# Optimization experiments

Measured on AMD Instinct MI355X. Metric: run time of the kernel, lower is better.

## Reference

```python
import jax, jax.numpy as jnp
import numpy as np

NUM_HEADS = 16
NUM_KV_HEADS = 4
HEAD_DIM = 128
SCALE = 0.08838834764831845  # 1/sqrt(128)
BATCH = 4
SEQLEN = 1024
TOTAL = BATCH * SEQLEN


def setup_inputs() -> dict:
    key = jax.random.key(0)
    kq, kk, kv = jax.random.split(key, 3)
    q = jax.random.normal(kq, (TOTAL, NUM_HEADS, HEAD_DIM), dtype=jnp.float32)
    k = jax.random.normal(kk, (TOTAL, NUM_KV_HEADS, HEAD_DIM), dtype=jnp.float32)
    v = jax.random.normal(kv, (TOTAL, NUM_KV_HEADS, HEAD_DIM), dtype=jnp.float32)
    cu = jnp.arange(BATCH + 1, dtype=jnp.int32) * SEQLEN  # [0,1024,2048,3072,4096]
    return {"q": q, "k": k, "v": v, "cu_seqlens_q": cu, "cu_seqlens_k": cu}


def reference(q, k, v, cu_seqlens_q, cu_seqlens_k):
    # Prefill varlen causal attention (block_tables=None, empty kv cache).
    # Equal-length segments -> reshape packed tokens to [B, S, H, D].
    B = cu_seqlens_q.shape[0] - 1
    S = q.shape[0] // B
    H, Dh = q.shape[1], q.shape[2]
    Hkv = k.shape[1]
    g = H // Hkv  # GQA group size

    qb = q.reshape(B, S, H, Dh)
    # repeat_interleave kv heads to match query heads
    kb = jnp.repeat(k.reshape(B, S, Hkv, Dh), g, axis=2)  # [B,S,H,Dh]
    vb = jnp.repeat(v.reshape(B, S, Hkv, Dh), g, axis=2)

    scores = jnp.einsum('bqhd,bkhd->bhqk', qb, kb) * SCALE  # [B,H,S,S]
    causal = jnp.tril(jnp.ones((S, S), dtype=bool))
    scores = jnp.where(causal, scores, jnp.finfo(scores.dtype).min)
    probs = jax.nn.softmax(scores, axis=-1)
    o = jnp.einsum('bhqk,bkhd->bqhd', probs, vb)  # [B,S,H,Dh]
    return o.reshape(B * S, H, Dh)
```

## Files before the change

### kernel.cpp

```cpp
#include <hip/hip_runtime.h>
#include <cstddef>

#define NH 16
#define NKV 4
#define HD 128
#define SEQ 1024
#define SCALE_F 0.08838834764831845f
#define QSCALE 0.12751743f

typedef __attribute__((ext_vector_type(8))) short short8;
typedef __attribute__((ext_vector_type(4))) float floatx4;

union F8 { short8 v; unsigned short u[8]; };

__device__ __forceinline__ unsigned short f2bf(float f) {
  unsigned int u = __float_as_uint(f);
  u += 0x7FFFu + ((u >> 16) & 1u);
  return (unsigned short)(u >> 16);
}

__device__ __forceinline__ unsigned int pk_bf16(float lo, float hi) {
  unsigned int r;
  asm("v_cvt_pk_bf16_f32 %0, %1, %2" : "=v"(r) : "v"(lo), "v"(hi));
  return r;
}

__device__ __forceinline__ void glds16(const void* g, void* l) {
  __builtin_amdgcn_global_load_lds(
      (const __attribute__((address_space(1))) unsigned int*)g,
      (__attribute__((address_space(3))) unsigned int*)l, 16, 0, 0);
}

__global__ __launch_bounds__(256) void prepass(const float* __restrict__ kg,
                                               const float* __restrict__ vg,
                                               unsigned short* __restrict__ Ktg,
                                               unsigned short* __restrict__ Vtg) {
  __shared__ float Vl[32 * 132];
  const int tid = threadIdx.x;
  const int bid = blockIdx.x;
  if (bid < 512) {
    const int bkvh = bid >> 5, tile = bid & 31;
    const int b = bkvh >> 2, kvh = bkvh & 3;
    const int kpos = tid >> 3;
    const int d8base = (tid & 7) * 2;
    const size_t tok = (size_t)b * SEQ + tile * 32 + kpos;
    const float* src = kg + (tok * NKV + kvh) * HD + d8base * 8;
    unsigned short* dstT = Ktg + (size_t)bid * 4096;
#pragma unroll
    for (int i = 0; i < 2; ++i) {
      floatx4 a = ((const floatx4*)src)[0];
      floatx4 c = ((const floatx4*)src)[1];
      F8 t;
#pragma unroll
      for (int j = 0; j < 4; ++j) { t.u[j] = f2bf(a[j]); t.u[4 + j] = f2bf(c[j]); }
      const int blk = kpos * 16 + ((d8base + i) ^ (kpos & 15));
      *(short8*)(dstT + blk * 8) = t.v;
      src += 8;
    }
  } else {
    const int bb = bid - 512;
    const int bkvh = bb >> 5, tile = bb & 31;
    const int b = bkvh >> 2, kvh = bkvh & 3;
    const int r = tid >> 3;
    const int c16 = (tid & 7) * 16;
    const size_t tok = (size_t)b * SEQ + tile * 32 + r;
    const float* src = vg + (tok * NKV + kvh) * HD + c16;
#pragma unroll
    for (int j = 0; j < 4; ++j)
      *(floatx4*)&Vl[r * 132 + c16 + j * 4] = ((const floatx4*)src)[j];
    __syncthreads();
    unsigned short* dstT = Vtg + (size_t)bb * 4096;
#pragma unroll
    for (int i = 0; i < 2; ++i) {
      const int o = tid * 2 + i;
      const int d = o >> 2, s8 = o & 3;
      F8 t;
#pragma unroll
      for (int j = 0; j < 8; ++j) {
        const int s = s8 * 8 + j;
        const int k = (s >> 1) + ((s & 1) << 4);
        t.u[j] = f2bf(Vl[k * 132 + d]);
      }
      const int blk = d * 4 + (s8 ^ (d & 3));
      *(short8*)(dstT + blk * 8) = t.v;
    }
  }
}

__global__ __launch_bounds__(256, 4)
void fa_fwd7(const float* __restrict__ qg, const unsigned short* __restrict__ Ktg,
             const unsigned short* __restrict__ Vtg, float* __restrict__ og) {
  __shared__ __align__(16) unsigned short Kb[2][4096];
  __shared__ __align__(16) unsigned int Pb[4][16 * 20];

  const int tid = threadIdx.x;
  const int wave = tid >> 6;
  const int lane = tid & 63;
  const int col = lane & 15;
  const int quad = lane >> 4;

  const int idx = blockIdx.x;
  const int g = idx >> 8;
  const int u = (idx >> 6) & 3;
  const int bh = idx & 63;
  const int qt = g * 4 + ((u + g) & 3);
  const int h = bh & 15;
  const int b = bh >> 4;
  const int kvh = h >> 2;
  const int seg = b * SEQ;
  const int wq0 = qt * 64 + wave * 16;
  const int tb = (b * NKV + kvh) * 32;

  F8 qf[4];
  {
    const float* qp = qg + ((size_t)(seg + wq0 + col) * NH + h) * HD + quad * 8;
#pragma unroll
    for (int ks = 0; ks < 4; ++ks) {
      floatx4 a = ((const floatx4*)(qp + ks * 32))[0];
      floatx4 c = ((const floatx4*)(qp + ks * 32))[1];
#pragma unroll
      for (int j = 0; j < 4; ++j) {
        qf[ks].u[j] = f2bf(a[j] * QSCALE);
        qf[ks].u[4 + j] = f2bf(c[j] * QSCALE);
      }
    }
  }

  floatx4 acc[8];
#pragma unroll
  for (int dt = 0; dt < 8; ++dt) acc[dt] = (floatx4){0.f, 0.f, 0.f, 0.f};
  float lsum[4] = {0.f, 0.f, 0.f, 0.f};

  const int nkt = 2 * (qt + 1);
  const int stoff = wave * 2048 + lane * 16;

  {
    const char* gK = (const char*)Ktg + (size_t)tb * 8192 + stoff;
    char* lK = (char*)&Kb[0][0] + wave * 2048;
    glds16(gK, lK);
    glds16(gK + 1024, lK + 1024);
  }
  __syncthreads();

  for (int kt = 0; kt < nkt; ++kt) {
    const int cb = kt & 1, nb = cb ^ 1;
    const int kbase = kt * 32;
    const bool act = (kbase <= wq0 + 15);

    F8 vr[8];
    if (act) {
      const unsigned short* Vt = Vtg + (size_t)(tb + kt) * 4096;
#pragma unroll
      for (int dt = 0; dt < 8; ++dt)
        vr[dt].v = *(const short8*)&Vt[((dt * 16 + col) * 4 + (quad ^ (col & 3))) * 8];
    }

    if (kt + 1 < nkt) {
      const char* gK = (const char*)Ktg + (size_t)(tb + kt + 1) * 8192 + stoff;
      char* lK = (char*)&Kb[nb][0] + wave * 2048;
      glds16(gK, lK);
      glds16(gK + 1024, lK + 1024);
    }

    if (act) {
      floatx4 s0 = {0.f, 0.f, 0.f, 0.f}, s1 = {0.f, 0.f, 0.f, 0.f};
#pragma unroll
      for (int ks = 0; ks < 4; ++ks) {
        F8 k0, k1;
        k0.v = *(const short8*)&Kb[cb][(col * 16 + ((ks * 4 + quad) ^ col)) * 8];
        k1.v = *(const short8*)&Kb[cb][((16 + col) * 16 + ((ks * 4 + quad) ^ col)) * 8];
        s0 = __builtin_amdgcn_mfma_f32_16x16x32_bf16(qf[ks].v, k0.v, s0, 0, 0, 0);
        s1 = __builtin_amdgcn_mfma_f32_16x16x32_bf16(qf[ks].v, k1.v, s1, 0, 0, 0);
      }
      const bool diag = (kbase + 31 > wq0);
#pragma unroll
      for (int r = 0; r < 4; ++r) {
        float p0 = __builtin_amdgcn_exp2f(s0[r]);
        float p1 = __builtin_amdgcn_exp2f(s1[r]);
        if (diag) {
          const int q0 = wq0 + quad * 4 + r;
          p0 = (kbase + col > q0) ? 0.f : p0;
          p1 = (kbase + 16 + col > q0) ? 0.f : p1;
        }
        lsum[r] += p0 + p1;
        Pb[wave][(quad * 4 + r) * 20 + col] = pk_bf16(p0, p1);
      }
      F8 pa;
      pa.v = *(const short8*)&Pb[wave][col * 20 + quad * 4];
#pragma unroll
      for (int dt = 0; dt < 8; ++dt)
        acc[dt] = __builtin_amdgcn_mfma_f32_16x16x32_bf16(pa.v, vr[dt].v, acc[dt], 0, 0, 0);
    }
    __syncthreads();
  }

#pragma unroll
  for (int r = 0; r < 4; ++r) {
    float l = lsum[r];
    l += __shfl_xor(l, 1);
    l += __shfl_xor(l, 2);
    l += __shfl_xor(l, 4);
    l += __shfl_xor(l, 8);
    const float inv = 1.0f / l;
    float* op = og + ((size_t)(seg + wq0 + quad * 4 + r) * NH + h) * HD;
#pragma unroll
    for (int dt = 0; dt < 8; ++dt) op[dt * 16 + col] = acc[dt][r] * inv;
  }
}

#define KST 136
#define VST 40
#define PST 40

__global__ __launch_bounds__(256, 2)
void fa_fwd(const float* __restrict__ qg, const float* __restrict__ kg,
            const float* __restrict__ vg, float* __restrict__ og) {
  __shared__ unsigned short Klds[32 * KST];
  __shared__ unsigned short Vt[HD * VST];
  __shared__ unsigned short Pl[4][32 * PST];

  const int tid = threadIdx.x;
  const int wave = tid >> 6;
  const int lane = tid & 63;
  const int col = lane & 15;
  const int quad = lane >> 4;

  const int idx = blockIdx.x;
  const int raw = idx & 7;
  const int qt = (idx & 256) ? raw : 7 - raw;
  const int bh = idx >> 3;
  const int h = bh & 15;
  const int b = bh >> 4;
  const int kvh = h >> 2;
  const int seg = b * SEQ;
  const int wq0 = qt * 128 + wave * 32;

  F8 qf[2][4];
#pragma unroll
  for (int mt = 0; mt < 2; ++mt) {
    const size_t qrow = (size_t)(seg + wq0 + mt * 16 + col);
    const float* qp = qg + (qrow * NH + h) * HD + quad * 8;
#pragma unroll
    for (int ks = 0; ks < 4; ++ks) {
      const floatx4* p4 = (const floatx4*)(qp + ks * 32);
      floatx4 a = p4[0], c = p4[1];
#pragma unroll
      for (int j = 0; j < 4; ++j) {
        qf[mt][ks].u[j] = f2bf(a[j] * SCALE_F);
        qf[mt][ks].u[4 + j] = f2bf(c[j] * SCALE_F);
      }
    }
  }

  floatx4 acc[2][8];
#pragma unroll
  for (int mt = 0; mt < 2; ++mt)
#pragma unroll
    for (int dt = 0; dt < 8; ++dt)
      acc[mt][dt] = (floatx4){0.f, 0.f, 0.f, 0.f};
  float lsum[2][4];
#pragma unroll
  for (int mt = 0; mt < 2; ++mt)
#pragma unroll
    for (int r = 0; r < 4; ++r) lsum[mt][r] = 0.f;

  const int nkt = 4 * (qt + 1);
  const int sr = tid >> 3;
  const int sc = (tid & 7) * 16;

  for (int kt = 0; kt < nkt; ++kt) {
    const int kbase = kt * 32;
    __syncthreads();
    {
      const size_t tok = (size_t)(seg + kbase + sr);
      const floatx4* kp4 = (const floatx4*)(kg + (tok * NKV + kvh) * HD + sc);
      floatx4 kv0 = kp4[0], kv1 = kp4[1], kv2 = kp4[2], kv3 = kp4[3];
      float kf32[16] = {kv0[0],kv0[1],kv0[2],kv0[3], kv1[0],kv1[1],kv1[2],kv1[3],
                        kv2[0],kv2[1],kv2[2],kv2[3], kv3[0],kv3[1],kv3[2],kv3[3]};
      unsigned int* dst = (unsigned int*)&Klds[sr * KST + sc];
#pragma unroll
      for (int j = 0; j < 8; ++j)
        dst[j] = (unsigned int)f2bf(kf32[2 * j]) | ((unsigned int)f2bf(kf32[2 * j + 1]) << 16);
      const floatx4* vp4 = (const floatx4*)(vg + (tok * NKV + kvh) * HD + sc);
      floatx4 vv0 = vp4[0], vv1 = vp4[1], vv2 = vp4[2], vv3 = vp4[3];
      unsigned short vb[16] = {
        f2bf(vv0[0]),f2bf(vv0[1]),f2bf(vv0[2]),f2bf(vv0[3]),
        f2bf(vv1[0]),f2bf(vv1[1]),f2bf(vv1[2]),f2bf(vv1[3]),
        f2bf(vv2[0]),f2bf(vv2[1]),f2bf(vv2[2]),f2bf(vv2[3]),
        f2bf(vv3[0]),f2bf(vv3[1]),f2bf(vv3[2]),f2bf(vv3[3])};
#pragma unroll
      for (int s = 0; s < 16; ++s) {
        int j = (s + tid) & 15;
        Vt[(sc + j) * VST + sr] = vb[j];
      }
    }
    __syncthreads();

    if (kbase > wq0 + 31) continue;

    F8 kf[4][2];
#pragma unroll
    for (int ks = 0; ks < 4; ++ks)
#pragma unroll
      for (int nt = 0; nt < 2; ++nt)
        kf[ks][nt].v = *(const short8*)&Klds[(nt * 16 + col) * KST + ks * 32 + quad * 8];

#pragma unroll
    for (int mt = 0; mt < 2; ++mt) {
      floatx4 s0 = {0.f, 0.f, 0.f, 0.f}, s1 = {0.f, 0.f, 0.f, 0.f};
#pragma unroll
      for (int ks = 0; ks < 4; ++ks) {
        s0 = __builtin_amdgcn_mfma_f32_16x16x32_bf16(qf[mt][ks].v, kf[ks][0].v, s0, 0, 0, 0);
        s1 = __builtin_amdgcn_mfma_f32_16x16x32_bf16(qf[mt][ks].v, kf[ks][1].v, s1, 0, 0, 0);
      }
      const int q0 = wq0 + mt * 16 + quad * 4;
      const bool diag = (kbase + 31 > wq0 + mt * 16);
      unsigned short* pw = &Pl[wave][(mt * 16 + quad * 4) * PST];
#pragma unroll
      for (int r = 0; r < 4; ++r) {
        float p0 = __expf(s0[r]);
        float p1 = __expf(s1[r]);
        if (diag) {
          p0 = (kbase + col > q0 + r) ? 0.f : p0;
          p1 = (kbase + 16 + col > q0 + r) ? 0.f : p1;
        }
        lsum[mt][r] += p0 + p1;
        pw[r * PST + col] = f2bf(p0);
        pw[r * PST + 16 + col] = f2bf(p1);
      }
    }
    F8 pa[2];
#pragma unroll
    for (int mt = 0; mt < 2; ++mt)
      pa[mt].v = *(const short8*)&Pl[wave][(mt * 16 + col) * PST + quad * 8];
#pragma unroll
    for (int dt = 0; dt < 8; ++dt) {
      F8 vb;
      vb.v = *(const short8*)&Vt[(dt * 16 + col) * VST + quad * 8];
#pragma unroll
      for (int mt = 0; mt < 2; ++mt)
        acc[mt][dt] = __builtin_amdgcn_mfma_f32_16x16x32_bf16(pa[mt].v, vb.v, acc[mt][dt], 0, 0, 0);
    }
  }

#pragma unroll
  for (int mt = 0; mt < 2; ++mt) {
#pragma unroll
    for (int r = 0; r < 4; ++r) {
      float l = lsum[mt][r];
      l += __shfl_xor(l, 1);
      l += __shfl_xor(l, 2);
      l += __shfl_xor(l, 4);
      l += __shfl_xor(l, 8);
      const float inv = 1.0f / l;
      const int qi = wq0 + mt * 16 + quad * 4 + r;
      float* op = og + ((size_t)(seg + qi) * NH + h) * HD;
#pragma unroll
      for (int dt = 0; dt < 8; ++dt)
        op[dt * 16 + col] = acc[mt][dt][r] * inv;
    }
  }
}

extern "C" void kernel_launch(void* const* d_in, const int* in_sizes, int n_in,
                              void* d_out, int out_size, void* d_ws, size_t ws_size,
                              hipStream_t stream) {
  const float* q = (const float*)d_in[0];
  const float* k = (const float*)d_in[1];
  const float* v = (const float*)d_in[2];
  float* out = (float*)d_out;
  if (ws_size >= (size_t)(8 * 1024 * 1024)) {
    unsigned short* Ktg = (unsigned short*)d_ws;
    unsigned short* Vtg = Ktg + 2097152;
    hipLaunchKernelGGL(prepass, dim3(1024), dim3(256), 0, stream, k, v, Ktg, Vtg);
    hipLaunchKernelGGL(fa_fwd7, dim3(1024), dim3(256), 0, stream, q, Ktg, Vtg, out);
  } else {
    hipLaunchKernelGGL(fa_fwd, dim3(512), dim3(256), 0, stream, q, k, v, out);
  }
}
```

Measured before the change: 129.1 us.

## Split long causal query tiles across two blocks with a normalization pass

Adds a split-K variant in which query tiles 8-15 are each handled by two blocks covering halves of the key range. Partial unnormalized outputs and row sums go to workspace, and a separate kernel combines and normalizes them. The goal is to balance per-block work under the causal mask and add more blocks for better occupancy. In exchange it needs extra global traffic for the partials, a third kernel launch, and a larger workspace requirement, so it only runs when the workspace is at least 26 MB.

```diff
diff --git a/kernel.cpp b/kernel.cpp
--- a/kernel.cpp
+++ b/kernel.cpp
@@ -88,6 +88,176 @@
 }
 
 __global__ __launch_bounds__(256, 4)
+void fa_fwd9(const float* __restrict__ qg, const unsigned short* __restrict__ Ktg,
+             const unsigned short* __restrict__ Vtg, float* __restrict__ og,
+             float* __restrict__ Pacc, float* __restrict__ Ls0,
+             float* __restrict__ Ls1) {
+  __shared__ __align__(16) unsigned short Kb[2][4096];
+  __shared__ __align__(16) unsigned int Pb[4][16 * 20];
+
+  const int tid = threadIdx.x;
+  const int wave = tid >> 6;
+  const int lane = tid & 63;
+  const int col = lane & 15;
+  const int quad = lane >> 4;
+
+  const int idx = blockIdx.x;
+  const int bh = idx & 63;
+  const int j = idx >> 6;
+  const int h = bh & 15;
+  const int b = bh >> 4;
+  const int kvh = h >> 2;
+  const int seg = b * SEQ;
+  const int tb = (b * NKV + kvh) * 32;
+
+  int qt, k0, k1, mode;
+  if (j < 8) {
+    qt = j; k0 = 0; k1 = 2 * (qt + 1); mode = 0;
+  } else {
+    const int s = j - 8;
+    qt = 8 + (s >> 1);
+    if ((s & 1) == 0) { k0 = 0;      k1 = qt + 1;       mode = 1; }
+    else              { k0 = qt + 1; k1 = 2 * (qt + 1); mode = 2; }
+  }
+  const int wq0 = qt * 64 + wave * 16;
+
+  F8 qf[4];
+  {
+    const float* qp = qg + ((size_t)(seg + wq0 + col) * NH + h) * HD + quad * 8;
+#pragma unroll
+    for (int ks = 0; ks < 4; ++ks) {
+      floatx4 a = ((const floatx4*)(qp + ks * 32))[0];
+      floatx4 c = ((const floatx4*)(qp + ks * 32))[1];
+#pragma unroll
+      for (int jj = 0; jj < 4; ++jj) {
+        qf[ks].u[jj] = f2bf(a[jj] * QSCALE);
+        qf[ks].u[4 + jj] = f2bf(c[jj] * QSCALE);
+      }
+    }
+  }
+
+  floatx4 acc[8];
+#pragma unroll
+  for (int dt = 0; dt < 8; ++dt) acc[dt] = (floatx4){0.f, 0.f, 0.f, 0.f};
+  float lsum[4] = {0.f, 0.f, 0.f, 0.f};
+
+  const int stoff = wave * 2048 + lane * 16;
+
+  {
+    const char* gK = (const char*)Ktg + (size_t)(tb + k0) * 8192 + stoff;
+    char* lK = (char*)&Kb[0][0] + wave * 2048;
+    glds16(gK, lK);
+    glds16(gK + 1024, lK + 1024);
+  }
+  __syncthreads();
+
+  for (int kt = k0; kt < k1; ++kt) {
+    const int cb = (kt - k0) & 1, nb = cb ^ 1;
+    const int kbase = kt * 32;
+    const bool act = (kbase <= wq0 + 15);
+
+    F8 vr[8];
+    if (act) {
+      const unsigned short* Vt = Vtg + (size_t)(tb + kt) * 4096;
+#pragma unroll
+      for (int dt = 0; dt < 8; ++dt)
+        vr[dt].v = *(const short8*)&Vt[((dt * 16 + col) * 4 + (quad ^ (col & 3))) * 8];
+    }
+
+    if (kt + 1 < k1) {
+      const char* gK = (const char*)Ktg + (size_t)(tb + kt + 1) * 8192 + stoff;
+      char* lK = (char*)&Kb[nb][0] + wave * 2048;
+      glds16(gK, lK);
+      glds16(gK + 1024, lK + 1024);
+    }
+
+    if (act) {
+      floatx4 s0 = {0.f, 0.f, 0.f, 0.f}, s1 = {0.f, 0.f, 0.f, 0.f};
+#pragma unroll
+      for (int ks = 0; ks < 4; ++ks) {
+        F8 kk0, kk1;
+        kk0.v = *(const short8*)&Kb[cb][(col * 16 + ((ks * 4 + quad) ^ col)) * 8];
+        kk1.v = *(const short8*)&Kb[cb][((16 + col) * 16 + ((ks * 4 + quad) ^ col)) * 8];
+        s0 = __builtin_amdgcn_mfma_f32_16x16x32_bf16(qf[ks].v, kk0.v, s0, 0, 0, 0);
+        s1 = __builtin_amdgcn_mfma_f32_16x16x32_bf16(qf[ks].v, kk1.v, s1, 0, 0, 0);
+      }
+      const bool diag = (kbase + 31 > wq0);
+#pragma unroll
+      for (int r = 0; r < 4; ++r) {
+        float p0 = __builtin_amdgcn_exp2f(s0[r]);
+        float p1 = __builtin_amdgcn_exp2f(s1[r]);
+        if (diag) {
+          const int q0 = wq0 + quad * 4 + r;
+          p0 = (kbase + col > q0) ? 0.f : p0;
+          p1 = (kbase + 16 + col > q0) ? 0.f : p1;
+        }
+        lsum[r] += p0 + p1;
+        Pb[wave][(quad * 4 + r) * 20 + col] = pk_bf16(p0, p1);
+      }
+      F8 pa;
+      pa.v = *(const short8*)&Pb[wave][col * 20 + quad * 4];
+#pragma unroll
+      for (int dt = 0; dt < 8; ++dt)
+        acc[dt] = __builtin_amdgcn_mfma_f32_16x16x32_bf16(pa.v, vr[dt].v, acc[dt], 0, 0, 0);
+    }
+    __syncthreads();
+  }
+
+#pragma unroll
+  for (int r = 0; r < 4; ++r) {
+    float l = lsum[r];
+    l += __shfl_xor(l, 1);
+    l += __shfl_xor(l, 2);
+    l += __shfl_xor(l, 4);
+    l += __shfl_xor(l, 8);
+    if (mode == 0) {
+      const float inv = 1.0f / l;
+      float* op = og + ((size_t)(seg + wq0 + quad * 4 + r) * NH + h) * HD;
+#pragma unroll
+      for (int dt = 0; dt < 8; ++dt) op[dt * 16 + col] = acc[dt][r] * inv;
+    } else {
+      const int roff = (qt - 8) * 64 + wave * 16 + quad * 4 + r;
+      const int lrow = (b * NH + h) * 512 + roff;
+      if (mode == 1) {
+        float* pp = Pacc + (size_t)lrow * 128;
+#pragma unroll
+        for (int dt = 0; dt < 8; ++dt) pp[dt * 16 + col] = acc[dt][r];
+        if (col == 0) Ls0[lrow] = l;
+      } else {
+        float* op = og + ((size_t)(seg + wq0 + quad * 4 + r) * NH + h) * HD;
+#pragma unroll
+        for (int dt = 0; dt < 8; ++dt) op[dt * 16 + col] = acc[dt][r];
+        if (col == 0) Ls1[lrow] = l;
+      }
+    }
+  }
+}
+
+__global__ __launch_bounds__(256)
+void norm_k(float* __restrict__ og, const float* __restrict__ Pacc,
+            const float* __restrict__ Ls0, const float* __restrict__ Ls1) {
+  const int t = blockIdx.x * 256 + threadIdx.x;
+  const int e = t * 8;
+  const int lrow = e >> 7;
+  const int d = e & 127;
+  const float inv = 1.0f / (Ls0[lrow] + Ls1[lrow]);
+  const int b = lrow >> 13;
+  const int rem = lrow & 8191;
+  const int h = rem >> 9;
+  const int roff = rem & 511;
+  float* op = og + (((size_t)(b * 1024 + 512 + roff) * NH + h) * HD + d);
+  const float* pp = Pacc + (size_t)lrow * 128 + d;
+#pragma unroll
+  for (int i = 0; i < 2; ++i) {
+    floatx4 o = ((floatx4*)op)[i];
+    floatx4 p = ((const floatx4*)pp)[i];
+#pragma unroll
+    for (int k = 0; k < 4; ++k) o[k] = (o[k] + p[k]) * inv;
+    ((floatx4*)op)[i] = o;
+  }
+}
+
+__global__ __launch_bounds__(256, 4)
 void fa_fwd7(const float* __restrict__ qg, const unsigned short* __restrict__ Ktg,
              const unsigned short* __restrict__ Vtg, float* __restrict__ og) {
   __shared__ __align__(16) unsigned short Kb[2][4096];
@@ -119,9 +289,9 @@
       floatx4 a = ((const floatx4*)(qp + ks * 32))[0];
       floatx4 c = ((const floatx4*)(qp + ks * 32))[1];
 #pragma unroll
-      for (int j = 0; j < 4; ++j) {
-        qf[ks].u[j] = f2bf(a[j] * QSCALE);
-        qf[ks].u[4 + j] = f2bf(c[j] * QSCALE);
+      for (int jj = 0; jj < 4; ++jj) {
+        qf[ks].u[jj] = f2bf(a[jj] * QSCALE);
+        qf[ks].u[4 + jj] = f2bf(c[jj] * QSCALE);
       }
     }
   }
@@ -166,11 +336,11 @@
       floatx4 s0 = {0.f, 0.f, 0.f, 0.f}, s1 = {0.f, 0.f, 0.f, 0.f};
 #pragma unroll
       for (int ks = 0; ks < 4; ++ks) {
-        F8 k0, k1;
-        k0.v = *(const short8*)&Kb[cb][(col * 16 + ((ks * 4 + quad) ^ col)) * 8];
-        k1.v = *(const short8*)&Kb[cb][((16 + col) * 16 + ((ks * 4 + quad) ^ col)) * 8];
-        s0 = __builtin_amdgcn_mfma_f32_16x16x32_bf16(qf[ks].v, k0.v, s0, 0, 0, 0);
-        s1 = __builtin_amdgcn_mfma_f32_16x16x32_bf16(qf[ks].v, k1.v, s1, 0, 0, 0);
+        F8 kk0, kk1;
+        kk0.v = *(const short8*)&Kb[cb][(col * 16 + ((ks * 4 + quad) ^ col)) * 8];
+        kk1.v = *(const short8*)&Kb[cb][((16 + col) * 16 + ((ks * 4 + quad) ^ col)) * 8];
+        s0 = __builtin_amdgcn_mfma_f32_16x16x32_bf16(qf[ks].v, kk0.v, s0, 0, 0, 0);
+        s1 = __builtin_amdgcn_mfma_f32_16x16x32_bf16(qf[ks].v, kk1.v, s1, 0, 0, 0);
       }
       const bool diag = (kbase + 31 > wq0);
 #pragma unroll
@@ -245,9 +415,9 @@
       const floatx4* p4 = (const floatx4*)(qp + ks * 32);
       floatx4 a = p4[0], c = p4[1];
 #pragma unroll
-      for (int j = 0; j < 4; ++j) {
-        qf[mt][ks].u[j] = f2bf(a[j] * SCALE_F);
-        qf[mt][ks].u[4 + j] = f2bf(c[j] * SCALE_F);
+      for (int jj = 0; jj < 4; ++jj) {
+        qf[mt][ks].u[jj] = f2bf(a[jj] * SCALE_F);
+        qf[mt][ks].u[4 + jj] = f2bf(c[jj] * SCALE_F);
       }
     }
   }
@@ -279,8 +449,8 @@
                         kv2[0],kv2[1],kv2[2],kv2[3], kv3[0],kv3[1],kv3[2],kv3[3]};
       unsigned int* dst = (unsigned int*)&Klds[sr * KST + sc];
 #pragma unroll
-      for (int j = 0; j < 8; ++j)
-        dst[j] = (unsigned int)f2bf(kf32[2 * j]) | ((unsigned int)f2bf(kf32[2 * j + 1]) << 16);
+      for (int jj = 0; jj < 8; ++jj)
+        dst[jj] = (unsigned int)f2bf(kf32[2 * jj]) | ((unsigned int)f2bf(kf32[2 * jj + 1]) << 16);
       const floatx4* vp4 = (const floatx4*)(vg + (tok * NKV + kvh) * HD + sc);
       floatx4 vv0 = vp4[0], vv1 = vp4[1], vv2 = vp4[2], vv3 = vp4[3];
       unsigned short vb[16] = {
@@ -290,8 +460,8 @@
         f2bf(vv3[0]),f2bf(vv3[1]),f2bf(vv3[2]),f2bf(vv3[3])};
 #pragma unroll
       for (int s = 0; s < 16; ++s) {
-        int j = (s + tid) & 15;
-        Vt[(sc + j) * VST + sr] = vb[j];
+        int jj = (s + tid) & 15;
+        Vt[(sc + jj) * VST + sr] = vb[jj];
       }
     }
     __syncthreads();
@@ -369,7 +539,18 @@
   const float* k = (const float*)d_in[1];
   const float* v = (const float*)d_in[2];
   float* out = (float*)d_out;
-  if (ws_size >= (size_t)(8 * 1024 * 1024)) {
+  const size_t MB = 1024 * 1024;
+  if (ws_size >= 26 * MB) {
+    unsigned short* Ktg = (unsigned short*)d_ws;
+    unsigned short* Vtg = Ktg + 2097152;
+    float* Pacc = (float*)((char*)d_ws + 8 * MB);
+    float* Ls0 = (float*)((char*)d_ws + 24 * MB);
+    float* Ls1 = Ls0 + 32768;
+    hipLaunchKernelGGL(prepass, dim3(1024), dim3(256), 0, stream, k, v, Ktg, Vtg);
+    hipLaunchKernelGGL(fa_fwd9, dim3(1536), dim3(256), 0, stream, q, Ktg, Vtg,
+                       out, Pacc, Ls0, Ls1);
+    hipLaunchKernelGGL(norm_k, dim3(2048), dim3(256), 0, stream, out, Pacc, Ls0, Ls1);
+  } else if (ws_size >= 8 * MB) {
     unsigned short* Ktg = (unsigned short*)d_ws;
     unsigned short* Vtg = Ktg + 2097152;
     hipLaunchKernelGGL(prepass, dim3(1024), dim3(256), 0, stream, k, v, Ktg, Vtg);
```

New measurement: 139.8 us. 8.3% more time.

## Read K fragments directly from global memory, dropping LDS staging and block barriers

Applied to the files above, without the earlier changes.

The main attention kernel stops staging K tiles into double-buffered shared memory through global_load_lds. Each wave now loads its K MFMA fragments straight from the pre-swizzled bf16 workspace, and V as before. Because waves no longer share a buffer, the per-iteration __syncthreads is removed and each wave runs only as many key tiles as its own causal rows need. This also skips the idle barrier iterations of early waves. The trade-off is that every wave reads K from global memory or cache separately instead of once per block, so K traffic rises and load latency is no longer overlapped through a prefetch.

```diff
diff --git a/kernel.cpp b/kernel.cpp
--- a/kernel.cpp
+++ b/kernel.cpp
@@ -23,12 +23,6 @@
   unsigned int r;
   asm("v_cvt_pk_bf16_f32 %0, %1, %2" : "=v"(r) : "v"(lo), "v"(hi));
   return r;
-}
-
-__device__ __forceinline__ void glds16(const void* g, void* l) {
-  __builtin_amdgcn_global_load_lds(
-      (const __attribute__((address_space(1))) unsigned int*)g,
-      (__attribute__((address_space(3))) unsigned int*)l, 16, 0, 0);
 }
 
 __global__ __launch_bounds__(256) void prepass(const float* __restrict__ kg,
@@ -88,9 +82,8 @@
 }
 
 __global__ __launch_bounds__(256, 4)
-void fa_fwd7(const float* __restrict__ qg, const unsigned short* __restrict__ Ktg,
-             const unsigned short* __restrict__ Vtg, float* __restrict__ og) {
-  __shared__ __align__(16) unsigned short Kb[2][4096];
+void fa_fwd10(const float* __restrict__ qg, const unsigned short* __restrict__ Ktg,
+              const unsigned short* __restrict__ Vtg, float* __restrict__ og) {
   __shared__ __align__(16) unsigned int Pb[4][16 * 20];
 
   const int tid = threadIdx.x;
@@ -131,67 +124,50 @@
   for (int dt = 0; dt < 8; ++dt) acc[dt] = (floatx4){0.f, 0.f, 0.f, 0.f};
   float lsum[4] = {0.f, 0.f, 0.f, 0.f};
 
-  const int nkt = 2 * (qt + 1);
-  const int stoff = wave * 2048 + lane * 16;
-
-  {
-    const char* gK = (const char*)Ktg + (size_t)tb * 8192 + stoff;
-    char* lK = (char*)&Kb[0][0] + wave * 2048;
-    glds16(gK, lK);
-    glds16(gK + 1024, lK + 1024);
-  }
-  __syncthreads();
-
-  for (int kt = 0; kt < nkt; ++kt) {
-    const int cb = kt & 1, nb = cb ^ 1;
+  const int nktw = ((wq0 + 15) >> 5) + 1;
+
+  int koff[4];
+#pragma unroll
+  for (int ks = 0; ks < 4; ++ks) koff[ks] = (col * 16 + ((ks * 4 + quad) ^ col)) * 8;
+  const int voffbase = (quad ^ (col & 3)) * 8;
+
+  for (int kt = 0; kt < nktw; ++kt) {
     const int kbase = kt * 32;
-    const bool act = (kbase <= wq0 + 15);
+    const unsigned short* Kt = Ktg + (size_t)(tb + kt) * 4096;
+    const unsigned short* Vt = Vtg + (size_t)(tb + kt) * 4096;
 
     F8 vr[8];
-    if (act) {
-      const unsigned short* Vt = Vtg + (size_t)(tb + kt) * 4096;
-#pragma unroll
-      for (int dt = 0; dt < 8; ++dt)
-        vr[dt].v = *(const short8*)&Vt[((dt * 16 + col) * 4 + (quad ^ (col & 3))) * 8];
-    }
-
-    if (kt + 1 < nkt) {
-      const char* gK = (const char*)Ktg + (size_t)(tb + kt + 1) * 8192 + stoff;
-      char* lK = (char*)&Kb[nb][0] + wave * 2048;
-      glds16(gK, lK);
-      glds16(gK + 1024, lK + 1024);
-    }
-
-    if (act) {
-      floatx4 s0 = {0.f, 0.f, 0.f, 0.f}, s1 = {0.f, 0.f, 0.f, 0.f};
-#pragma unroll
-      for (int ks = 0; ks < 4; ++ks) {
-        F8 k0, k1;
-        k0.v = *(const short8*)&Kb[cb][(col * 16 + ((ks * 4 + quad) ^ col)) * 8];
-        k1.v = *(const short8*)&Kb[cb][((16 + col) * 16 + ((ks * 4 + quad) ^ col)) * 8];
-        s0 = __builtin_amdgcn_mfma_f32_16x16x32_bf16(qf[ks].v, k0.v, s0, 0, 0, 0);
-        s1 = __builtin_amdgcn_mfma_f32_16x16x32_bf16(qf[ks].v, k1.v, s1, 0, 0, 0);
-      }
-      const bool diag = (kbase + 31 > wq0);
-#pragma unroll
-      for (int r = 0; r < 4; ++r) {
-        float p0 = __builtin_amdgcn_exp2f(s0[r]);
-        float p1 = __builtin_amdgcn_exp2f(s1[r]);
-        if (diag) {
-          const int q0 = wq0 + quad * 4 + r;
-          p0 = (kbase + col > q0) ? 0.f : p0;
-          p1 = (kbase + 16 + col > q0) ? 0.f : p1;
-        }
-        lsum[r] += p0 + p1;
-        Pb[wave][(quad * 4 + r) * 20 + col] = pk_bf16(p0, p1);
-      }
-      F8 pa;
-      pa.v = *(const short8*)&Pb[wave][col * 20 + quad * 4];
-#pragma unroll
-      for (int dt = 0; dt < 8; ++dt)
-        acc[dt] = __builtin_amdgcn_mfma_f32_16x16x32_bf16(pa.v, vr[dt].v, acc[dt], 0, 0, 0);
-    }
-    __syncthreads();
+#pragma unroll
+    for (int dt = 0; dt < 8; ++dt)
+      vr[dt].v = *(const short8*)&Vt[(dt * 16 + col) * 32 + voffbase];
+
+    floatx4 s0 = {0.f, 0.f, 0.f, 0.f}, s1 = {0.f, 0.f, 0.f, 0.f};
+#pragma unroll
+    for (int ks = 0; ks < 4; ++ks) {
+      F8 k0, k1;
+      k0.v = *(const short8*)&Kt[koff[ks]];
+      k1.v = *(const short8*)&Kt[16 * 16 * 8 + koff[ks]];
+      s0 = __builtin_amdgcn_mfma_f32_16x16x32_bf16(qf[ks].v, k0.v, s0, 0, 0, 0);
+      s1 = __builtin_amdgcn_mfma_f32_16x16x32_bf16(qf[ks].v, k1.v, s1, 0, 0, 0);
+    }
+    const bool diag = (kbase + 31 > wq0);
+#pragma unroll
+    for (int r = 0; r < 4; ++r) {
+      float p0 = __builtin_amdgcn_exp2f(s0[r]);
+      float p1 = __builtin_amdgcn_exp2f(s1[r]);
+      if (diag) {
+        const int q0 = wq0 + quad * 4 + r;
+        p0 = (kbase + col > q0) ? 0.f : p0;
+        p1 = (kbase + 16 + col > q0) ? 0.f : p1;
+      }
+      lsum[r] += p0 + p1;
+      Pb[wave][(quad * 4 + r) * 20 + col] = pk_bf16(p0, p1);
+    }
+    F8 pa;
+    pa.v = *(const short8*)&Pb[wave][col * 20 + quad * 4];
+#pragma unroll
+    for (int dt = 0; dt < 8; ++dt)
+      acc[dt] = __builtin_amdgcn_mfma_f32_16x16x32_bf16(pa.v, vr[dt].v, acc[dt], 0, 0, 0);
   }
 
 #pragma unroll
@@ -245,9 +221,9 @@
       const floatx4* p4 = (const floatx4*)(qp + ks * 32);
       floatx4 a = p4[0], c = p4[1];
 #pragma unroll
-      for (int j = 0; j < 4; ++j) {
-        qf[mt][ks].u[j] = f2bf(a[j] * SCALE_F);
-        qf[mt][ks].u[4 + j] = f2bf(c[j] * SCALE_F);
+      for (int jj = 0; jj < 4; ++jj) {
+        qf[mt][ks].u[jj] = f2bf(a[jj] * SCALE_F);
+        qf[mt][ks].u[4 + jj] = f2bf(c[jj] * SCALE_F);
       }
     }
   }
@@ -279,8 +255,8 @@
                         kv2[0],kv2[1],kv2[2],kv2[3], kv3[0],kv3[1],kv3[2],kv3[3]};
       unsigned int* dst = (unsigned int*)&Klds[sr * KST + sc];
 #pragma unroll
-      for (int j = 0; j < 8; ++j)
-        dst[j] = (unsigned int)f2bf(kf32[2 * j]) | ((unsigned int)f2bf(kf32[2 * j + 1]) << 16);
+      for (int jj = 0; jj < 8; ++jj)
+        dst[jj] = (unsigned int)f2bf(kf32[2 * jj]) | ((unsigned int)f2bf(kf32[2 * jj + 1]) << 16);
       const floatx4* vp4 = (const floatx4*)(vg + (tok * NKV + kvh) * HD + sc);
       floatx4 vv0 = vp4[0], vv1 = vp4[1], vv2 = vp4[2], vv3 = vp4[3];
       unsigned short vb[16] = {
@@ -290,8 +266,8 @@
         f2bf(vv3[0]),f2bf(vv3[1]),f2bf(vv3[2]),f2bf(vv3[3])};
 #pragma unroll
       for (int s = 0; s < 16; ++s) {
-        int j = (s + tid) & 15;
-        Vt[(sc + j) * VST + sr] = vb[j];
+        int jj = (s + tid) & 15;
+        Vt[(sc + jj) * VST + sr] = vb[jj];
       }
     }
     __syncthreads();
@@ -373,7 +349,7 @@
     unsigned short* Ktg = (unsigned short*)d_ws;
     unsigned short* Vtg = Ktg + 2097152;
     hipLaunchKernelGGL(prepass, dim3(1024), dim3(256), 0, stream, k, v, Ktg, Vtg);
-    hipLaunchKernelGGL(fa_fwd7, dim3(1024), dim3(256), 0, stream, q, Ktg, Vtg, out);
+    hipLaunchKernelGGL(fa_fwd10, dim3(1024), dim3(256), 0, stream, q, Ktg, Vtg, out);
   } else {
     hipLaunchKernelGGL(fa_fwd, dim3(512), dim3(256), 0, stream, q, k, v, out);
   }
```

Result: slower. 154.5 us (+19.7%).

## Process two 16-row query tiles per wave to reuse K/V fragments

Applied to the files above, without the earlier changes.

Each wave now handles 32 query rows as two 16-row sub-tiles, A and B. The K fragments read from LDS and the V fragments read from global memory are shared between both sub-tiles, so the block covers 128 query rows and the grid is halved to 512 blocks. The block-to-tile mapping changes to interleave even and odd super-tiles for causal load balance. The cost is doubled accumulator and register pressure, and launch bounds drop to 2 blocks per SM, which lowers occupancy.

```diff
diff --git a/kernel.cpp b/kernel.cpp
--- a/kernel.cpp
+++ b/kernel.cpp
@@ -87,11 +87,12 @@
   }
 }
 
-__global__ __launch_bounds__(256, 4)
-void fa_fwd7(const float* __restrict__ qg, const unsigned short* __restrict__ Ktg,
-             const unsigned short* __restrict__ Vtg, float* __restrict__ og) {
+__global__ __launch_bounds__(256, 2)
+void fa_fwd11(const float* __restrict__ qg, const unsigned short* __restrict__ Ktg,
+              const unsigned short* __restrict__ Vtg, float* __restrict__ og) {
   __shared__ __align__(16) unsigned short Kb[2][4096];
-  __shared__ __align__(16) unsigned int Pb[4][16 * 20];
+  __shared__ __align__(16) unsigned int PbA[4][320];
+  __shared__ __align__(16) unsigned int PbB[4][320];
 
   const int tid = threadIdx.x;
   const int wave = tid >> 6;
@@ -100,103 +101,139 @@
   const int quad = lane >> 4;
 
   const int idx = blockIdx.x;
-  const int g = idx >> 8;
-  const int u = (idx >> 6) & 3;
   const int bh = idx & 63;
-  const int qt = g * 4 + ((u + g) & 3);
+  const int st = (idx < 256) ? 2 * (idx >> 6) : 2 * ((idx - 256) >> 6) + 1;
   const int h = bh & 15;
   const int b = bh >> 4;
   const int kvh = h >> 2;
   const int seg = b * SEQ;
-  const int wq0 = qt * 64 + wave * 16;
+  const int wq0 = st * 128 + wave * 32;
   const int tb = (b * NKV + kvh) * 32;
-
-  F8 qf[4];
+  const int nkt = 4 * (st + 1);
+
+  F8 qfA[4], qfB[4];
   {
-    const float* qp = qg + ((size_t)(seg + wq0 + col) * NH + h) * HD + quad * 8;
+    const float* qpA = qg + ((size_t)(seg + wq0 + col) * NH + h) * HD + quad * 8;
+    const float* qpB = qg + ((size_t)(seg + wq0 + 16 + col) * NH + h) * HD + quad * 8;
 #pragma unroll
     for (int ks = 0; ks < 4; ++ks) {
-      floatx4 a = ((const floatx4*)(qp + ks * 32))[0];
-      floatx4 c = ((const floatx4*)(qp + ks * 32))[1];
+      floatx4 a = ((const floatx4*)(qpA + ks * 32))[0];
+      floatx4 c = ((const floatx4*)(qpA + ks * 32))[1];
 #pragma unroll
       for (int j = 0; j < 4; ++j) {
-        qf[ks].u[j] = f2bf(a[j] * QSCALE);
-        qf[ks].u[4 + j] = f2bf(c[j] * QSCALE);
-      }
-    }
-  }
-
-  floatx4 acc[8];
-#pragma unroll
-  for (int dt = 0; dt < 8; ++dt) acc[dt] = (floatx4){0.f, 0.f, 0.f, 0.f};
-  float lsum[4] = {0.f, 0.f, 0.f, 0.f};
-
-  const int nkt = 2 * (qt + 1);
+        qfA[ks].u[j] = f2bf(a[j] * QSCALE);
+        qfA[ks].u[4 + j] = f2bf(c[j] * QSCALE);
+      }
+      a = ((const floatx4*)(qpB + ks * 32))[0];
+      c = ((const floatx4*)(qpB + ks * 32))[1];
+#pragma unroll
+      for (int j = 0; j < 4; ++j) {
+        qfB[ks].u[j] = f2bf(a[j] * QSCALE);
+        qfB[ks].u[4 + j] = f2bf(c[j] * QSCALE);
+      }
+    }
+  }
+
+  floatx4 accA[8], accB[8];
+#pragma unroll
+  for (int dt = 0; dt < 8; ++dt) {
+    accA[dt] = (floatx4){0.f, 0.f, 0.f, 0.f};
+    accB[dt] = (floatx4){0.f, 0.f, 0.f, 0.f};
+  }
+  float lsumA[4] = {0.f, 0.f, 0.f, 0.f};
+  float lsumB[4] = {0.f, 0.f, 0.f, 0.f};
+
   const int stoff = wave * 2048 + lane * 16;
 
-  {
-    const char* gK = (const char*)Ktg + (size_t)tb * 8192 + stoff;
-    char* lK = (char*)&Kb[0][0] + wave * 2048;
-    glds16(gK, lK);
-    glds16(gK + 1024, lK + 1024);
-  }
+#define STAGE(T, BUF)                                                       \
+  do {                                                                      \
+    const char* gK_ = (const char*)Ktg + (size_t)(tb + (T)) * 8192 + stoff; \
+    char* lK_ = (char*)&Kb[BUF][0] + wave * 2048;                           \
+    glds16(gK_, lK_);                                                       \
+    glds16(gK_ + 1024, lK_ + 1024);                                         \
+  } while (0)
+
+  STAGE(0, 0);
   __syncthreads();
 
   for (int kt = 0; kt < nkt; ++kt) {
     const int cb = kt & 1, nb = cb ^ 1;
     const int kbase = kt * 32;
-    const bool act = (kbase <= wq0 + 15);
+    const bool actA = (kbase <= wq0 + 15);
+    const bool actB = (kbase <= wq0 + 31);
 
     F8 vr[8];
-    if (act) {
+    if (actB) {
       const unsigned short* Vt = Vtg + (size_t)(tb + kt) * 4096;
 #pragma unroll
       for (int dt = 0; dt < 8; ++dt)
         vr[dt].v = *(const short8*)&Vt[((dt * 16 + col) * 4 + (quad ^ (col & 3))) * 8];
     }
 
-    if (kt + 1 < nkt) {
-      const char* gK = (const char*)Ktg + (size_t)(tb + kt + 1) * 8192 + stoff;
-      char* lK = (char*)&Kb[nb][0] + wave * 2048;
-      glds16(gK, lK);
-      glds16(gK + 1024, lK + 1024);
-    }
-
-    if (act) {
-      floatx4 s0 = {0.f, 0.f, 0.f, 0.f}, s1 = {0.f, 0.f, 0.f, 0.f};
+    if (kt + 1 < nkt) STAGE(kt + 1, nb);
+
+    if (actB) {
+      floatx4 sA0 = {0.f, 0.f, 0.f, 0.f}, sA1 = {0.f, 0.f, 0.f, 0.f};
+      floatx4 sB0 = {0.f, 0.f, 0.f, 0.f}, sB1 = {0.f, 0.f, 0.f, 0.f};
 #pragma unroll
       for (int ks = 0; ks < 4; ++ks) {
         F8 k0, k1;
         k0.v = *(const short8*)&Kb[cb][(col * 16 + ((ks * 4 + quad) ^ col)) * 8];
         k1.v = *(const short8*)&Kb[cb][((16 + col) * 16 + ((ks * 4 + quad) ^ col)) * 8];
-        s0 = __builtin_amdgcn_mfma_f32_16x16x32_bf16(qf[ks].v, k0.v, s0, 0, 0, 0);
-        s1 = __builtin_amdgcn_mfma_f32_16x16x32_bf16(qf[ks].v, k1.v, s1, 0, 0, 0);
-      }
-      const bool diag = (kbase + 31 > wq0);
-#pragma unroll
-      for (int r = 0; r < 4; ++r) {
-        float p0 = __builtin_amdgcn_exp2f(s0[r]);
-        float p1 = __builtin_amdgcn_exp2f(s1[r]);
-        if (diag) {
-          const int q0 = wq0 + quad * 4 + r;
-          p0 = (kbase + col > q0) ? 0.f : p0;
-          p1 = (kbase + 16 + col > q0) ? 0.f : p1;
+        sB0 = __builtin_amdgcn_mfma_f32_16x16x32_bf16(qfB[ks].v, k0.v, sB0, 0, 0, 0);
+        sB1 = __builtin_amdgcn_mfma_f32_16x16x32_bf16(qfB[ks].v, k1.v, sB1, 0, 0, 0);
+        if (actA) {
+          sA0 = __builtin_amdgcn_mfma_f32_16x16x32_bf16(qfA[ks].v, k0.v, sA0, 0, 0, 0);
+          sA1 = __builtin_amdgcn_mfma_f32_16x16x32_bf16(qfA[ks].v, k1.v, sA1, 0, 0, 0);
         }
-        lsum[r] += p0 + p1;
-        Pb[wave][(quad * 4 + r) * 20 + col] = pk_bf16(p0, p1);
-      }
-      F8 pa;
-      pa.v = *(const short8*)&Pb[wave][col * 20 + quad * 4];
-#pragma unroll
-      for (int dt = 0; dt < 8; ++dt)
-        acc[dt] = __builtin_amdgcn_mfma_f32_16x16x32_bf16(pa.v, vr[dt].v, acc[dt], 0, 0, 0);
+      }
+      {
+        const bool diag = (kbase + 31 > wq0 + 16);
+#pragma unroll
+        for (int r = 0; r < 4; ++r) {
+          float p0 = __builtin_amdgcn_exp2f(sB0[r]);
+          float p1 = __builtin_amdgcn_exp2f(sB1[r]);
+          if (diag) {
+            const int q0 = wq0 + 16 + quad * 4 + r;
+            p0 = (kbase + col > q0) ? 0.f : p0;
+            p1 = (kbase + 16 + col > q0) ? 0.f : p1;
+          }
+          lsumB[r] += p0 + p1;
+          PbB[wave][(quad * 4 + r) * 20 + col] = pk_bf16(p0, p1);
+        }
+      }
+      if (actA) {
+        const bool diag = (kbase + 31 > wq0);
+#pragma unroll
+        for (int r = 0; r < 4; ++r) {
+          float p0 = __builtin_amdgcn_exp2f(sA0[r]);
+          float p1 = __builtin_amdgcn_exp2f(sA1[r]);
+          if (diag) {
+            const int q0 = wq0 + quad * 4 + r;
+            p0 = (kbase + col > q0) ? 0.f : p0;
+            p1 = (kbase + 16 + col > q0) ? 0.f : p1;
+          }
+          lsumA[r] += p0 + p1;
+          PbA[wave][(quad * 4 + r) * 20 + col] = pk_bf16(p0, p1);
+        }
+      }
+      F8 paB, paA;
+      paB.v = *(const short8*)&PbB[wave][col * 20 + quad * 4];
+      if (actA) paA.v = *(const short8*)&PbA[wave][col * 20 + quad * 4];
+#pragma unroll
+      for (int dt = 0; dt < 8; ++dt) {
+        accB[dt] = __builtin_amdgcn_mfma_f32_16x16x32_bf16(paB.v, vr[dt].v, accB[dt], 0, 0, 0);
+        if (actA)
+          accA[dt] = __builtin_amdgcn_mfma_f32_16x16x32_bf16(paA.v, vr[dt].v, accA[dt], 0, 0, 0);
+      }
     }
     __syncthreads();
   }
+#undef STAGE
 
 #pragma unroll
   for (int r = 0; r < 4; ++r) {
-    float l = lsum[r];
+    float l = lsumA[r];
     l += __shfl_xor(l, 1);
     l += __shfl_xor(l, 2);
     l += __shfl_xor(l, 4);
@@ -204,7 +241,19 @@
     const float inv = 1.0f / l;
     float* op = og + ((size_t)(seg + wq0 + quad * 4 + r) * NH + h) * HD;
 #pragma unroll
-    for (int dt = 0; dt < 8; ++dt) op[dt * 16 + col] = acc[dt][r] * inv;
+    for (int dt = 0; dt < 8; ++dt) op[dt * 16 + col] = accA[dt][r] * inv;
+  }
+#pragma unroll
+  for (int r = 0; r < 4; ++r) {
+    float l = lsumB[r];
+    l += __shfl_xor(l, 1);
+    l += __shfl_xor(l, 2);
+    l += __shfl_xor(l, 4);
+    l += __shfl_xor(l, 8);
+    const float inv = 1.0f / l;
+    float* op = og + ((size_t)(seg + wq0 + 16 + quad * 4 + r) * NH + h) * HD;
+#pragma unroll
+    for (int dt = 0; dt < 8; ++dt) op[dt * 16 + col] = accB[dt][r] * inv;
   }
 }
 
@@ -245,9 +294,9 @@
       const floatx4* p4 = (const floatx4*)(qp + ks * 32);
       floatx4 a = p4[0], c = p4[1];
 #pragma unroll
-      for (int j = 0; j < 4; ++j) {
-        qf[mt][ks].u[j] = f2bf(a[j] * SCALE_F);
-        qf[mt][ks].u[4 + j] = f2bf(c[j] * SCALE_F);
+      for (int jj = 0; jj < 4; ++jj) {
+        qf[mt][ks].u[jj] = f2bf(a[jj] * SCALE_F);
+        qf[mt][ks].u[4 + jj] = f2bf(c[jj] * SCALE_F);
       }
     }
   }
@@ -279,8 +328,8 @@
                         kv2[0],kv2[1],kv2[2],kv2[3], kv3[0],kv3[1],kv3[2],kv3[3]};
       unsigned int* dst = (unsigned int*)&Klds[sr * KST + sc];
 #pragma unroll
-      for (int j = 0; j < 8; ++j)
-        dst[j] = (unsigned int)f2bf(kf32[2 * j]) | ((unsigned int)f2bf(kf32[2 * j + 1]) << 16);
+      for (int jj = 0; jj < 8; ++jj)
+        dst[jj] = (unsigned int)f2bf(kf32[2 * jj]) | ((unsigned int)f2bf(kf32[2 * jj + 1]) << 16);
       const floatx4* vp4 = (const floatx4*)(vg + (tok * NKV + kvh) * HD + sc);
       floatx4 vv0 = vp4[0], vv1 = vp4[1], vv2 = vp4[2], vv3 = vp4[3];
       unsigned short vb[16] = {
@@ -290,8 +339,8 @@
         f2bf(vv3[0]),f2bf(vv3[1]),f2bf(vv3[2]),f2bf(vv3[3])};
 #pragma unroll
       for (int s = 0; s < 16; ++s) {
-        int j = (s + tid) & 15;
-        Vt[(sc + j) * VST + sr] = vb[j];
+        int jj = (s + tid) & 15;
+        Vt[(sc + jj) * VST + sr] = vb[jj];
       }
     }
     __syncthreads();
@@ -373,7 +422,7 @@
     unsigned short* Ktg = (unsigned short*)d_ws;
     unsigned short* Vtg = Ktg + 2097152;
     hipLaunchKernelGGL(prepass, dim3(1024), dim3(256), 0, stream, k, v, Ktg, Vtg);
-    hipLaunchKernelGGL(fa_fwd7, dim3(1024), dim3(256), 0, stream, q, Ktg, Vtg, out);
+    hipLaunchKernelGGL(fa_fwd11, dim3(512), dim3(256), 0, stream, q, Ktg, Vtg, out);
   } else {
     hipLaunchKernelGGL(fa_fwd, dim3(512), dim3(256), 0, stream, q, k, v, out);
   }
```

Measured after the change: 138.4 us. 7.3% more time.
